# Kernel tuning notes

Measured on AMD Instinct MI355X. Metric: run time of the kernel, lower is better.

## Reference

```python
import jax, jax.numpy as jnp
import numpy as np

N_TOKEN = 392
POS_WEIGHT = 1.0
LOSS_WEIGHT = 1.0


def _cam_map(logits, w_proj, xf, shape):
    # logits: (B, K_cls); w_proj: (K_cls, C); xf: (B, C, N)
    B, T, H, W = shape
    top_cls = jnp.argmax(logits, axis=1)                 # sort desc -> [0] == argmax
    w_top = w_proj[top_cls]                              # (B, C) gather top-class weight row
    row = jnp.einsum('bc,bcn->bn', w_top, xf)            # (B, N) per-sample CAM scores
    mn = row.min(axis=1, keepdims=True)
    mx = row.max(axis=1, keepdims=True)
    rown = (row - mn) / (mx - mn)                        # min-max normalize
    vals, idxs = jax.lax.top_k(rown, N_TOKEN)            # (B, 392)
    hw = H * W
    ti = idxs // hw
    hi = (idxs % hw) // W
    wi = idxs % W
    bi = jnp.broadcast_to(jnp.arange(B)[:, None], idxs.shape)
    cam = jnp.zeros((B, T, H, W), rown.dtype).at[bi, ti, hi, wi].set(vals)
    return cam


def _forward(x, pred_v_logits, pred_n_logits, w_proj_v, w_proj_n,
             conv_w, conv_b, score_w, score_b):
    B, C, T, H, W = x.shape
    xf = x.reshape(B, C, T * H * W)
    cam_v = _cam_map(pred_v_logits, w_proj_v, xf, (B, T, H, W))
    cam_n = _cam_map(pred_n_logits, w_proj_n, xf, (B, T, H, W))
    cam_gt = jnp.maximum(cam_v, cam_n)                   # torch.where(v > n, v, n)
    cam_gt = jax.lax.stop_gradient(cam_gt)               # original builds it from numpy + .detach()

    dn = ('NCDHW', 'OIDHW', 'NCDHW')
    h1 = jax.nn.relu(
        jax.lax.conv_general_dilated(x, conv_w, (1, 1, 1),
                                     [(0, 0), (1, 1), (1, 1)],
                                     dimension_numbers=dn)
        + conv_b[None, :, None, None, None])
    logits = (jax.lax.conv_general_dilated(h1, score_w, (1, 1, 1),
                                           [(0, 0), (0, 0), (0, 0)],
                                           dimension_numbers=dn)
              + score_b[None, :, None, None, None])      # (B,1,T,H,W)

    xcam = logits[:, 0].reshape(B * T, H * W)
    y = cam_gt.reshape(B * T, H * W)
    # BCEWithLogitsLoss(pos_weight) mean
    bce = -(POS_WEIGHT * y * jax.nn.log_sigmoid(xcam)
            + (1.0 - y) * jax.nn.log_sigmoid(-xcam))
    return LOSS_WEIGHT * bce.mean()


def setup_inputs() -> dict:
    key = jax.random.key(0)
    ks = jax.random.split(key, 8)
    B, C, T, H, W = 64, 256, 32, 7, 7
    Kv, Kn, D = 97, 300, 512
    x = jax.random.normal(ks[0], (B, C, T, H, W), jnp.float32)
    pred_v_logits = jax.random.normal(ks[1], (B, Kv), jnp.float32)
    pred_n_logits = jax.random.normal(ks[2], (B, Kn), jnp.float32)
    w_proj_v = jax.random.normal(ks[3], (Kv, C), jnp.float32) / np.sqrt(C)
    w_proj_n = jax.random.normal(ks[4], (Kn, C), jnp.float32) / np.sqrt(C)
    conv_w = jax.random.normal(ks[5], (D, C, 1, 3, 3), jnp.float32) / np.sqrt(C * 9)
    conv_b = jnp.zeros((D,), jnp.float32)
    score_w = jax.random.normal(ks[6], (1, D, 1, 1, 1), jnp.float32) / np.sqrt(D)
    score_b = jnp.zeros((1,), jnp.float32)
    return {"x": x, "pred_v_logits": pred_v_logits, "pred_n_logits": pred_n_logits,
            "w_proj_v": w_proj_v, "w_proj_n": w_proj_n,
            "conv_w": conv_w, "conv_b": conv_b,
            "score_w": score_w, "score_b": score_b}


def reference(x, pred_v_logits, pred_n_logits, w_proj_v, w_proj_n,
              conv_w, conv_b, score_w, score_b):
    return _forward(x, pred_v_logits, pred_n_logits, w_proj_v, w_proj_n,
                    conv_w, conv_b, score_w, score_b)
```

## Files before the change

kernel.cpp:

```cpp
#include <hip/hip_runtime.h>
#include <hip/hip_bf16.h>
#include <math.h>

#define BB 64
#define CC 256
#define TT 32
#define HH 7
#define WW 7
#define HW 49
#define NN 1568
#define KV 97
#define KN 300
#define DD 512
#define NTOK 392
#define TOTAL (BB*TT*HW)
#define BCAP 256

typedef float f32x4 __attribute__((ext_vector_type(4)));
typedef short bf16x8 __attribute__((ext_vector_type(8)));

#define GLDS(g, l) __builtin_amdgcn_global_load_lds(                          \
    (const __attribute__((address_space(1))) void*)(g),                       \
    (__attribute__((address_space(3))) void*)(l), 16, 0, 0)

__global__ void k_pre(const float* __restrict__ w, __hip_bfloat16* __restrict__ wb,
                      const float* __restrict__ pv, const float* __restrict__ pn,
                      int* __restrict__ clsv, int* __restrict__ clsn,
                      int* __restrict__ counter) {
    int blk = blockIdx.x;
    if (blk < 4608) {
        int o = blk * 256 + threadIdx.x;
        int kk = o / (DD * CC);
        int rem = o - kk * (DD * CC);
        int d = rem >> 8, c = rem & 255;
        wb[o] = __float2bfloat16(w[(d * CC + c) * 9 + kk]);
        return;
    }
    int tid = threadIdx.x;
    if (tid == 64) *counter = 0;
    if (tid >= BB) return;
    {
        const float* r = pv + tid * KV;
        float best = r[0]; int bi = 0;
        for (int k = 1; k < KV; ++k) { float v = r[k]; if (v > best) { best = v; bi = k; } }
        clsv[tid] = bi;
    }
    {
        const float* r = pn + tid * KN;
        float best = r[0]; int bi = 0;
        for (int k = 1; k < KN; ++k) { float v = r[k]; if (v > best) { best = v; bi = k; } }
        clsn[tid] = bi;
    }
}

__global__ __launch_bounds__(256) void k_xp(
        const float* __restrict__ x, __hip_bfloat16* __restrict__ xp,
        const float* __restrict__ wpv, const float* __restrict__ wpn,
        const int* __restrict__ clsv, const int* __restrict__ clsn,
        float* __restrict__ rowv, float* __restrict__ rown_) {
    __shared__ float xs[CC * HW];
    __shared__ float wvs[CC], wns[CC];
    __shared__ float psum[4 * HW];
    int bt = blockIdx.x;
    int b = bt >> 5, t = bt & 31;
    int tid = threadIdx.x;
    wvs[tid] = wpv[clsv[b] * CC + tid];
    wns[tid] = wpn[clsn[b] * CC + tid];
    const float* xb = x + ((size_t)b * CC * TT + t) * HW;
    for (int i = tid; i < CC * HW; i += 256) {
        int c = i / HW, q = i - (i / HW) * HW;
        xs[i] = xb[(size_t)c * (TT * HW) + q];
    }
    __syncthreads();
    __hip_bfloat16* xpb = xp + (size_t)bt * 81 * CC;
    for (int u = tid; u < 81 * 32; u += 256) {
        int p = u >> 5, c0 = (u & 31) * 8;
        int hh = p / 9, ww = p - (p / 9) * 9;
        bool inb = (hh >= 1 && hh <= 7 && ww >= 1 && ww <= 7);
        int base = c0 * HW + (hh - 1) * WW + (ww - 1);
        bf16x8 pack;
        #pragma unroll
        for (int j = 0; j < 8; ++j) {
            float v = inb ? xs[base + j * HW] : 0.f;
            __hip_bfloat16 bv = __float2bfloat16(v);
            pack[j] = *reinterpret_cast<short*>(&bv);
        }
        *reinterpret_cast<bf16x8*>(xpb + p * 256 + c0) = pack;
    }
    if (tid < 4 * HW) {
        int sel = tid / HW;
        int q = tid - sel * HW;
        const float* w = (sel < 2) ? wvs : wns;
        int cb2 = (sel & 1) * 128;
        float s = 0.f;
        #pragma unroll 4
        for (int c = 0; c < 128; ++c) s = fmaf(w[cb2 + c], xs[(cb2 + c) * HW + q], s);
        psum[tid] = s;
    }
    __syncthreads();
    if (tid < 2 * HW) {
        int head = tid >= HW;
        int q = head ? tid - HW : tid;
        float s = head ? (psum[2 * HW + q] + psum[3 * HW + q])
                       : (psum[q] + psum[HW + q]);
        (head ? rown_ : rowv)[bt * HW + q] = s;
    }
}

__device__ __forceinline__ int binof(float v) {
    int i = (int)(v * 1024.f);
    return i < 0 ? 0 : (i > 1023 ? 1023 : i);
}

__global__ __launch_bounds__(256) void k_cam(
        const float* __restrict__ rowv, const float* __restrict__ rown_,
        float* __restrict__ cam) {
    __shared__ float rv[NN], rn[NN];
    __shared__ float wred[4][4];
    __shared__ int h[1024];
    __shared__ int tsum[256];
    __shared__ float lval_v[BCAP], lval_n[BCAP];
    __shared__ int lidx_v[BCAP], lidx_n[BCAP];
    __shared__ int cntv, cntn, bstar_v, above_v, bstar_n, above_n;
    int b = blockIdx.x, tid = threadIdx.x;

    for (int n = tid; n < NN; n += 256) { rv[n] = rowv[b * NN + n]; rn[n] = rown_[b * NN + n]; }
    __syncthreads();
    float mnv = 1e30f, mxv = -1e30f, mnn = 1e30f, mxn = -1e30f;
    for (int n = tid; n < NN; n += 256) {
        float v = rv[n]; mnv = fminf(mnv, v); mxv = fmaxf(mxv, v);
        float u = rn[n]; mnn = fminf(mnn, u); mxn = fmaxf(mxn, u);
    }
    #pragma unroll
    for (int off = 32; off >= 1; off >>= 1) {
        mnv = fminf(mnv, __shfl_xor(mnv, off));
        mxv = fmaxf(mxv, __shfl_xor(mxv, off));
        mnn = fminf(mnn, __shfl_xor(mnn, off));
        mxn = fmaxf(mxn, __shfl_xor(mxn, off));
    }
    if ((tid & 63) == 0) {
        int wid = tid >> 6;
        wred[wid][0] = mnv; wred[wid][1] = mxv; wred[wid][2] = mnn; wred[wid][3] = mxn;
    }
    if (tid == 0) { cntv = 0; cntn = 0; }
    __syncthreads();
    mnv = fminf(fminf(wred[0][0], wred[1][0]), fminf(wred[2][0], wred[3][0]));
    mxv = fmaxf(fmaxf(wred[0][1], wred[1][1]), fmaxf(wred[2][1], wred[3][1]));
    mnn = fminf(fminf(wred[0][2], wred[1][2]), fminf(wred[2][2], wred[3][2]));
    mxn = fmaxf(fmaxf(wred[0][3], wred[1][3]), fmaxf(wred[2][3], wred[3][3]));
    float iv = 1.f / (mxv - mnv), inn = 1.f / (mxn - mnn);

    for (int n = tid; n < NN; n += 256) {
        rv[n] = (rv[n] - mnv) * iv;
        rn[n] = (rn[n] - mnn) * inn;
    }
    for (int i = tid; i < 1024; i += 256) h[i] = 0;
    __syncthreads();
    for (int n = tid; n < NN; n += 256) {
        atomicAdd(&h[binof(rv[n])], 1);
        atomicAdd(&h[binof(rn[n])], 1 << 16);
    }
    __syncthreads();

    int h0 = h[4 * tid], h1 = h[4 * tid + 1], h2 = h[4 * tid + 2], h3 = h[4 * tid + 3];
    tsum[tid] = h0 + h1 + h2 + h3;
    __syncthreads();
    for (int off = 1; off < 256; off <<= 1) {
        int add = (tid + off < 256) ? tsum[tid + off] : 0;
        __syncthreads();
        tsum[tid] += add;
        __syncthreads();
    }
    {
        int scur = tsum[tid];
        int hk[4] = {h0, h1, h2, h3};
        #pragma unroll
        for (int k = 0; k < 4; ++k) {
            int snext = scur - hk[k];
            int sc = scur & 0xffff, nc = snext & 0xffff;
            int sh = scur >> 16, nh = snext >> 16;
            if (sc >= NTOK && nc < NTOK) { bstar_v = 4 * tid + k; above_v = nc; }
            if (sh >= NTOK && nh < NTOK) { bstar_n = 4 * tid + k; above_n = nh; }
            scur = snext;
        }
    }
    __syncthreads();
    int bsv = bstar_v, abv = above_v, bsn = bstar_n, abn = above_n;

    for (int n = tid; n < NN; n += 256) {
        float v = rv[n]; int bv = binof(v);
        if (bv < bsv) rv[n] = 0.f;
        else if (bv == bsv) {
            int s = atomicAdd(&cntv, 1);
            if (s < BCAP) { lval_v[s] = v; lidx_v[s] = n; }
        }
        float u = rn[n]; int bu = binof(u);
        if (bu < bsn) rn[n] = 0.f;
        else if (bu == bsn) {
            int s = atomicAdd(&cntn, 1);
            if (s < BCAP) { lval_n[s] = u; lidx_n[s] = n; }
        }
    }
    __syncthreads();
    int Lv = cntv < BCAP ? cntv : BCAP;
    int Ln = cntn < BCAP ? cntn : BCAP;
    for (int i = tid; i < Lv; i += 256) {
        float vi = lval_v[i]; int ni = lidx_v[i]; int r = 0;
        for (int j = 0; j < Lv; ++j) {
            float vj = lval_v[j]; int nj = lidx_v[j];
            r += (vj > vi || (vj == vi && nj < ni)) ? 1 : 0;
        }
        rv[ni] = (r < NTOK - abv) ? vi : 0.f;
    }
    for (int i = tid; i < Ln; i += 256) {
        float vi = lval_n[i]; int ni = lidx_n[i]; int r = 0;
        for (int j = 0; j < Ln; ++j) {
            float vj = lval_n[j]; int nj = lidx_n[j];
            r += (vj > vi || (vj == vi && nj < ni)) ? 1 : 0;
        }
        rn[ni] = (r < NTOK - abn) ? vi : 0.f;
    }
    __syncthreads();
    for (int n = tid; n < NN; n += 256) cam[b * NN + n] = fmaxf(rv[n], rn[n]);
}

__global__ __launch_bounds__(256, 3) void k_gemm(
        const __hip_bfloat16* __restrict__ xp, const __hip_bfloat16* __restrict__ wb,
        const float* __restrict__ convb, const float* __restrict__ scorew,
        float* __restrict__ pl) {
    __shared__ char As[16384];
    __shared__ char Bs[16384];
    int tid = threadIdx.x;
    int bid = blockIdx.x;
    int xcd = bid & 7;
    int local = bid >> 3;
    int mtile = xcd * 98 + (local >> 2);
    int nblk = local & 3;
    int m0 = mtile * 128;
    int n0 = nblk * 128;
    int lane = tid & 63, wv = tid >> 6;
    int wm = wv >> 1, wn = wv & 1;
    int ln = lane & 15, qd = lane >> 4;

    int rrow = tid >> 3;
    int segst = ((tid & 7) ^ (rrow & 7)) * 8;
    int bt_[4], hh_[4], ww_[4];
    const __hip_bfloat16* bptr[4];
    #pragma unroll
    for (int j = 0; j < 4; ++j) {
        int m = m0 + j * 32 + rrow;
        int bt = m / HW, q = m - bt * HW;
        bt_[j] = bt; hh_[j] = q / WW; ww_[j] = q - (q / WW) * WW;
        bptr[j] = wb + (size_t)(n0 + j * 32 + rrow) * 256 + segst;
    }

    int swz = ln & 7;
    int offk[2] = {((0 + qd) ^ swz) * 16, ((4 + qd) ^ swz) * 16};

    f32x4 acc[4][4];
    #pragma unroll
    for (int i = 0; i < 4; ++i)
        #pragma unroll
        for (int j = 0; j < 4; ++j) acc[i][j] = (f32x4){0.f, 0.f, 0.f, 0.f};

    for (int kk = 0; kk < 9; ++kk) {
        int kh = kk / 3, kw = kk - (kk / 3) * 3;
        const __hip_bfloat16* aptr[4];
        #pragma unroll
        for (int j = 0; j < 4; ++j)
            aptr[j] = xp + ((size_t)bt_[j] * 81 + (hh_[j] + kh) * 9 + (ww_[j] + kw)) * 256 + segst;
        const size_t boff = (size_t)kk * (DD * 256);
        #pragma unroll
        for (int c0 = 0; c0 < 256; c0 += 64) {
            __syncthreads();
            #pragma unroll
            for (int j = 0; j < 4; ++j) {
                GLDS(aptr[j] + c0, As + j * 4096 + tid * 16);
                GLDS(bptr[j] + boff + c0, Bs + j * 4096 + tid * 16);
            }
            __syncthreads();
            #pragma unroll
            for (int k2 = 0; k2 < 2; ++k2) {
                bf16x8 af[4], bfr[4];
                #pragma unroll
                for (int i = 0; i < 4; ++i)
                    af[i] = *(const bf16x8*)(As + (wm * 64 + i * 16 + ln) * 128 + offk[k2]);
                #pragma unroll
                for (int j = 0; j < 4; ++j)
                    bfr[j] = *(const bf16x8*)(Bs + (wn * 64 + j * 16 + ln) * 128 + offk[k2]);
                #pragma unroll
                for (int i = 0; i < 4; ++i)
                    #pragma unroll
                    for (int j = 0; j < 4; ++j)
                        acc[i][j] = __builtin_amdgcn_mfma_f32_16x16x32_bf16(af[i], bfr[j], acc[i][j], 0, 0, 0);
            }
        }
    }

    float swr[4], cbr[4];
    #pragma unroll
    for (int j = 0; j < 4; ++j) {
        int n = n0 + wn * 64 + j * 16 + ln;
        swr[j] = scorew[n];
        cbr[j] = convb[n];
    }
    float* dst = pl + (size_t)(nblk * 2 + wn) * TOTAL;
    #pragma unroll
    for (int i = 0; i < 4; ++i) {
        #pragma unroll
        for (int r = 0; r < 4; ++r) {
            float v = 0.f;
            #pragma unroll
            for (int j = 0; j < 4; ++j) {
                float h1 = acc[i][j][r] + cbr[j];
                h1 = h1 > 0.f ? h1 : 0.f;
                v = fmaf(swr[j], h1, v);
            }
            v += __shfl_xor(v, 1);
            v += __shfl_xor(v, 2);
            v += __shfl_xor(v, 4);
            v += __shfl_xor(v, 8);
            if (ln == 0)
                dst[m0 + wm * 64 + i * 16 + qd * 4 + r] = v;
        }
    }
}

__global__ __launch_bounds__(256) void k_bce(
        const float* __restrict__ pl, const float* __restrict__ cam,
        const float* __restrict__ sb, float* __restrict__ part,
        int* __restrict__ counter, float* __restrict__ out) {
    __shared__ float sbuf[256];
    __shared__ int isLast;
    int tid = threadIdx.x;
    int m = blockIdx.x * 256 + tid;
    float l = sb[0];
    #pragma unroll
    for (int s = 0; s < 8; ++s) l += pl[(size_t)s * TOTAL + m];
    float y = cam[m];
    float v = fmaxf(l, 0.f) - l * y + log1pf(expf(-fabsf(l)));
    sbuf[tid] = v; __syncthreads();
    for (int k = 128; k > 0; k >>= 1) {
        if (tid < k) sbuf[tid] += sbuf[tid + k];
        __syncthreads();
    }
    if (tid == 0) {
        part[blockIdx.x] = sbuf[0];
        __threadfence();
        int d = atomicAdd(counter, 1);
        isLast = (d == 391);
    }
    __syncthreads();
    if (isLast) {
        float s = 0.f;
        for (int i = tid; i < 392; i += 256) s += part[i];
        sbuf[tid] = s; __syncthreads();
        for (int k = 128; k > 0; k >>= 1) {
            if (tid < k) sbuf[tid] += sbuf[tid + k];
            __syncthreads();
        }
        if (tid == 0) out[0] = sbuf[0] * (1.0f / (float)TOTAL);
    }
}

extern "C" void kernel_launch(void* const* d_in, const int* in_sizes, int n_in,
                              void* d_out, int out_size, void* d_ws, size_t ws_size,
                              hipStream_t stream) {
    const float* x   = (const float*)d_in[0];
    const float* pv  = (const float*)d_in[1];
    const float* pn  = (const float*)d_in[2];
    const float* wpv = (const float*)d_in[3];
    const float* wpn = (const float*)d_in[4];
    const float* cw  = (const float*)d_in[5];
    const float* cb  = (const float*)d_in[6];
    const float* sw  = (const float*)d_in[7];
    const float* sb  = (const float*)d_in[8];

    char* w8 = (char*)d_ws;
    __hip_bfloat16* xp  = (__hip_bfloat16*)w8;
    __hip_bfloat16* wb  = (__hip_bfloat16*)(w8 + 84934656);
    float* pl      = (float*)(w8 + 87293952);
    float* rowv    = (float*)(w8 + 90505216);
    float* rown_   = (float*)(w8 + 90906624);
    float* cam     = (float*)(w8 + 91308032);
    float* part    = (float*)(w8 + 91709440);
    int*   counter = (int*)(w8 + 91711008);
    int*   clsv    = (int*)(w8 + 91711016);
    int*   clsn    = clsv + 64;

    k_pre<<<4609, 256, 0, stream>>>(cw, wb, pv, pn, clsv, clsn, counter);
    k_xp<<<BB * TT, 256, 0, stream>>>(x, xp, wpv, wpn, clsv, clsn, rowv, rown_);
    k_cam<<<BB, 256, 0, stream>>>(rowv, rown_, cam);
    k_gemm<<<3136, 256, 0, stream>>>(xp, wb, cb, sw, pl);
    k_bce<<<392, 256, 0, stream>>>(pl, cam, sb, part, counter, (float*)d_out);
}
```

Before: 470.8 us.

## Fuse prep into k_xp and double GEMM M-tile to 256 rows

Three changes. The weight-conversion and argmax prep kernel is merged into k_xp: the class argmax is now computed per block with a wave reduction and the bf16 weight conversion runs in extra blocks. The counter reset moves into k_cam, which removes one launch. The GEMM tile grows from 128x128 to 256x128, with 8 A-row groups per block and twice the LDS for A, so each B tile is reused more; launch bounds drop to 2 blocks per SM. Each block now needs more registers (acc[8][4]) and fewer blocks can be resident, which lowers occupancy and may hurt latency hiding.

Result: slower. 569.3 us (+20.9%).

```diff
diff --git a/kernel.cpp b/kernel.cpp
--- a/kernel.cpp
+++ b/kernel.cpp
@@ -23,54 +23,55 @@
     (const __attribute__((address_space(1))) void*)(g),                       \
     (__attribute__((address_space(3))) void*)(l), 16, 0, 0)
 
-__global__ void k_pre(const float* __restrict__ w, __hip_bfloat16* __restrict__ wb,
-                      const float* __restrict__ pv, const float* __restrict__ pn,
-                      int* __restrict__ clsv, int* __restrict__ clsn,
-                      int* __restrict__ counter) {
+__global__ __launch_bounds__(256) void k_xp(
+        const float* __restrict__ x, __hip_bfloat16* __restrict__ xp,
+        const float* __restrict__ pv, const float* __restrict__ pn,
+        const float* __restrict__ wpv, const float* __restrict__ wpn,
+        const float* __restrict__ cw, __hip_bfloat16* __restrict__ wb,
+        float* __restrict__ rowv, float* __restrict__ rown_) {
     int blk = blockIdx.x;
-    if (blk < 4608) {
-        int o = blk * 256 + threadIdx.x;
+    int tid = threadIdx.x;
+    if (blk >= 2048) {
+        int o = (blk - 2048) * 256 + tid;
         int kk = o / (DD * CC);
         int rem = o - kk * (DD * CC);
         int d = rem >> 8, c = rem & 255;
-        wb[o] = __float2bfloat16(w[(d * CC + c) * 9 + kk]);
+        wb[o] = __float2bfloat16(cw[(d * CC + c) * 9 + kk]);
         return;
     }
-    int tid = threadIdx.x;
-    if (tid == 64) *counter = 0;
-    if (tid >= BB) return;
-    {
-        const float* r = pv + tid * KV;
-        float best = r[0]; int bi = 0;
-        for (int k = 1; k < KV; ++k) { float v = r[k]; if (v > best) { best = v; bi = k; } }
-        clsv[tid] = bi;
-    }
-    {
-        const float* r = pn + tid * KN;
-        float best = r[0]; int bi = 0;
-        for (int k = 1; k < KN; ++k) { float v = r[k]; if (v > best) { best = v; bi = k; } }
-        clsn[tid] = bi;
-    }
-}
-
-__global__ __launch_bounds__(256) void k_xp(
-        const float* __restrict__ x, __hip_bfloat16* __restrict__ xp,
-        const float* __restrict__ wpv, const float* __restrict__ wpn,
-        const int* __restrict__ clsv, const int* __restrict__ clsn,
-        float* __restrict__ rowv, float* __restrict__ rown_) {
     __shared__ float xs[CC * HW];
     __shared__ float wvs[CC], wns[CC];
     __shared__ float psum[4 * HW];
-    int bt = blockIdx.x;
+    __shared__ int cls_sh[2];
+    int bt = blk;
     int b = bt >> 5, t = bt & 31;
-    int tid = threadIdx.x;
-    wvs[tid] = wpv[clsv[b] * CC + tid];
-    wns[tid] = wpn[clsn[b] * CC + tid];
+    int lane = tid & 63;
+
+    if (tid < 128) {
+        int head = tid >> 6;
+        const float* r = head ? (pn + b * KN) : (pv + b * KV);
+        int K = head ? KN : KV;
+        float best = -1e30f; int bi = 0x7fffffff;
+        for (int k = lane; k < K; k += 64) {
+            float v = r[k];
+            if (v > best || (v == best && k < bi)) { best = v; bi = k; }
+        }
+        #pragma unroll
+        for (int off = 32; off >= 1; off >>= 1) {
+            float ov = __shfl_xor(best, off);
+            int oi = __shfl_xor(bi, off);
+            if (ov > best || (ov == best && oi < bi)) { best = ov; bi = oi; }
+        }
+        if (lane == 0) cls_sh[head] = bi;
+    }
     const float* xb = x + ((size_t)b * CC * TT + t) * HW;
     for (int i = tid; i < CC * HW; i += 256) {
         int c = i / HW, q = i - (i / HW) * HW;
         xs[i] = xb[(size_t)c * (TT * HW) + q];
     }
+    __syncthreads();
+    wvs[tid] = wpv[cls_sh[0] * CC + tid];
+    wns[tid] = wpn[cls_sh[1] * CC + tid];
     __syncthreads();
     __hip_bfloat16* xpb = xp + (size_t)bt * 81 * CC;
     for (int u = tid; u < 81 * 32; u += 256) {
@@ -114,7 +115,7 @@
 
 __global__ __launch_bounds__(256) void k_cam(
         const float* __restrict__ rowv, const float* __restrict__ rown_,
-        float* __restrict__ cam) {
+        float* __restrict__ cam, int* __restrict__ counter) {
     __shared__ float rv[NN], rn[NN];
     __shared__ float wred[4][4];
     __shared__ int h[1024];
@@ -123,6 +124,7 @@
     __shared__ int lidx_v[BCAP], lidx_n[BCAP];
     __shared__ int cntv, cntn, bstar_v, above_v, bstar_n, above_n;
     int b = blockIdx.x, tid = threadIdx.x;
+    if (b == 0 && tid == 0) *counter = 0;
 
     for (int n = tid; n < NN; n += 256) { rv[n] = rowv[b * NN + n]; rn[n] = rown_[b * NN + n]; }
     __syncthreads();
@@ -224,19 +226,19 @@
     for (int n = tid; n < NN; n += 256) cam[b * NN + n] = fmaxf(rv[n], rn[n]);
 }
 
-__global__ __launch_bounds__(256, 3) void k_gemm(
+__global__ __launch_bounds__(256, 2) void k_gemm(
         const __hip_bfloat16* __restrict__ xp, const __hip_bfloat16* __restrict__ wb,
         const float* __restrict__ convb, const float* __restrict__ scorew,
         float* __restrict__ pl) {
-    __shared__ char As[16384];
+    __shared__ char As[32768];
     __shared__ char Bs[16384];
     int tid = threadIdx.x;
     int bid = blockIdx.x;
     int xcd = bid & 7;
     int local = bid >> 3;
-    int mtile = xcd * 98 + (local >> 2);
+    int mtile = xcd * 49 + (local >> 2);
     int nblk = local & 3;
-    int m0 = mtile * 128;
+    int m0 = mtile * 256;
     int n0 = nblk * 128;
     int lane = tid & 63, wv = tid >> 6;
     int wm = wv >> 1, wn = wv & 1;
@@ -244,52 +246,55 @@
 
     int rrow = tid >> 3;
     int segst = ((tid & 7) ^ (rrow & 7)) * 8;
-    int bt_[4], hh_[4], ww_[4];
+    int bt_[8], hh_[8], ww_[8];
     const __hip_bfloat16* bptr[4];
     #pragma unroll
-    for (int j = 0; j < 4; ++j) {
+    for (int j = 0; j < 8; ++j) {
         int m = m0 + j * 32 + rrow;
         int bt = m / HW, q = m - bt * HW;
         bt_[j] = bt; hh_[j] = q / WW; ww_[j] = q - (q / WW) * WW;
+    }
+    #pragma unroll
+    for (int j = 0; j < 4; ++j)
         bptr[j] = wb + (size_t)(n0 + j * 32 + rrow) * 256 + segst;
-    }
 
     int swz = ln & 7;
     int offk[2] = {((0 + qd) ^ swz) * 16, ((4 + qd) ^ swz) * 16};
 
-    f32x4 acc[4][4];
-    #pragma unroll
-    for (int i = 0; i < 4; ++i)
+    f32x4 acc[8][4];
+    #pragma unroll
+    for (int i = 0; i < 8; ++i)
         #pragma unroll
         for (int j = 0; j < 4; ++j) acc[i][j] = (f32x4){0.f, 0.f, 0.f, 0.f};
 
     for (int kk = 0; kk < 9; ++kk) {
         int kh = kk / 3, kw = kk - (kk / 3) * 3;
-        const __hip_bfloat16* aptr[4];
-        #pragma unroll
-        for (int j = 0; j < 4; ++j)
+        const __hip_bfloat16* aptr[8];
+        #pragma unroll
+        for (int j = 0; j < 8; ++j)
             aptr[j] = xp + ((size_t)bt_[j] * 81 + (hh_[j] + kh) * 9 + (ww_[j] + kw)) * 256 + segst;
         const size_t boff = (size_t)kk * (DD * 256);
         #pragma unroll
         for (int c0 = 0; c0 < 256; c0 += 64) {
             __syncthreads();
             #pragma unroll
-            for (int j = 0; j < 4; ++j) {
+            for (int j = 0; j < 8; ++j)
                 GLDS(aptr[j] + c0, As + j * 4096 + tid * 16);
+            #pragma unroll
+            for (int j = 0; j < 4; ++j)
                 GLDS(bptr[j] + boff + c0, Bs + j * 4096 + tid * 16);
-            }
             __syncthreads();
             #pragma unroll
             for (int k2 = 0; k2 < 2; ++k2) {
-                bf16x8 af[4], bfr[4];
+                bf16x8 af[8], bfr[4];
                 #pragma unroll
-                for (int i = 0; i < 4; ++i)
-                    af[i] = *(const bf16x8*)(As + (wm * 64 + i * 16 + ln) * 128 + offk[k2]);
+                for (int i = 0; i < 8; ++i)
+                    af[i] = *(const bf16x8*)(As + (wm * 128 + i * 16 + ln) * 128 + offk[k2]);
                 #pragma unroll
                 for (int j = 0; j < 4; ++j)
                     bfr[j] = *(const bf16x8*)(Bs + (wn * 64 + j * 16 + ln) * 128 + offk[k2]);
                 #pragma unroll
-                for (int i = 0; i < 4; ++i)
+                for (int i = 0; i < 8; ++i)
                     #pragma unroll
                     for (int j = 0; j < 4; ++j)
                         acc[i][j] = __builtin_amdgcn_mfma_f32_16x16x32_bf16(af[i], bfr[j], acc[i][j], 0, 0, 0);
@@ -306,7 +311,7 @@
     }
     float* dst = pl + (size_t)(nblk * 2 + wn) * TOTAL;
     #pragma unroll
-    for (int i = 0; i < 4; ++i) {
+    for (int i = 0; i < 8; ++i) {
         #pragma unroll
         for (int r = 0; r < 4; ++r) {
             float v = 0.f;
@@ -321,7 +326,7 @@
             v += __shfl_xor(v, 4);
             v += __shfl_xor(v, 8);
             if (ln == 0)
-                dst[m0 + wm * 64 + i * 16 + qd * 4 + r] = v;
+                dst[m0 + wm * 128 + i * 16 + qd * 4 + r] = v;
         }
     }
 }
@@ -385,12 +390,9 @@
     float* cam     = (float*)(w8 + 91308032);
     float* part    = (float*)(w8 + 91709440);
     int*   counter = (int*)(w8 + 91711008);
-    int*   clsv    = (int*)(w8 + 91711016);
-    int*   clsn    = clsv + 64;
-
-    k_pre<<<4609, 256, 0, stream>>>(cw, wb, pv, pn, clsv, clsn, counter);
-    k_xp<<<BB * TT, 256, 0, stream>>>(x, xp, wpv, wpn, clsv, clsn, rowv, rown_);
-    k_cam<<<BB, 256, 0, stream>>>(rowv, rown_, cam);
-    k_gemm<<<3136, 256, 0, stream>>>(xp, wb, cb, sw, pl);
+
+    k_xp<<<2048 + 4608, 256, 0, stream>>>(x, xp, pv, pn, wpv, wpn, cw, wb, rowv, rown_);
+    k_cam<<<BB, 256, 0, stream>>>(rowv, rown_, cam, counter);
+    k_gemm<<<1568, 256, 0, stream>>>(xp, wb, cb, sw, pl);
     k_bce<<<392, 256, 0, stream>>>(pl, cam, sb, part, counter, (float*)d_out);
 }
```
